# Optimization experiments

Hardware: AMD Instinct MI355X
Metric: run time of the kernel (lower is better)

## Reference

```python
import jax, jax.numpy as jnp
import numpy as np

BATCH, IN_DIM, N_HID, OUT_DIM = 8192, 1024, 2048, 256
EDGE_DENSITY = 0.05


def _make_mat():
    # adjacency with activation-type codes: 0=no edge, 1=w*x, 2=relu(w*x), 3=tanh(w*x), 4=sigmoid(w*x)
    rng = np.random.default_rng(0)
    n_rows, n_cols = N_HID + OUT_DIM, IN_DIM + N_HID
    mat = rng.integers(1, 5, size=(n_rows, n_cols)) * (rng.random((n_rows, n_cols)) < EDGE_DENSITY)
    mat[:N_HID, IN_DIM:] = 0  # hidden nodes read only from inputs (valid DAG instance of the loop)
    # guarantee every node has at least one incoming edge (original code assumes this)
    hz = np.where(mat[:N_HID, :IN_DIM].sum(1) == 0)[0]
    mat[hz, hz % IN_DIM] = 1
    oz = np.where(mat[N_HID:].sum(1) == 0)[0]
    mat[N_HID + oz, oz % n_cols] = 1
    return mat.astype(np.int32)


def setup_inputs() -> dict:
    key = jax.random.key(0)
    x = jax.random.normal(key, (BATCH, IN_DIM), dtype=jnp.float32)
    w = jnp.ones((), dtype=jnp.float32)  # constant_weight
    mat = jnp.asarray(_make_mat())
    return {"x": x, "w": w, "mat": mat}


_ACTS = [(1, lambda z: z), (2, jax.nn.relu), (3, jnp.tanh), (4, jax.nn.sigmoid)]


def _node_values(src, w, M):
    # src: [B, S] source node values; M: [R, S] activation-type codes
    # node_r = sum_s act_{M[r,s]}(w * src[:, s]) for M[r,s] != 0
    total = jnp.zeros((src.shape[0], M.shape[0]), dtype=src.dtype)
    ws = w * src
    for t, f in _ACTS:
        mask = (M == t).astype(src.dtype)  # [R, S]
        total = total + f(ws) @ mask.T
    return total


def reference(x, w, mat):
    in_dim = x.shape[1]
    num_hidden = mat.shape[1] - in_dim
    hidden = _node_values(x, w, mat[:num_hidden, :in_dim])          # [B, N_HID]
    src = jnp.concatenate([x, hidden], axis=1)                       # [B, IN+N_HID]
    outputs = _node_values(src, w, mat[num_hidden:, :])              # [B, OUT]
    return outputs
```

## Files before the change

kernel.cpp:

```cpp
#include <hip/hip_runtime.h>
#include <hip/hip_bf16.h>
#include <stdint.h>

#define BATCH   8192
#define IN_DIM  1024
#define N_HID   2048
#define OUT_DIM 256
#define SRC_DIM 3072

#define C     32
#define RB    16
#define BT    256
#define S1_CH (IN_DIM / C)
#define S1_RB (N_HID / RB)
#define S2_CH (SRC_DIM / C)
#define S2_RB (OUT_DIM / RB)
#define NSEG1 (S1_RB * S1_CH)
#define NSEG2 (S2_RB * S2_CH)
#define NCG2  16
#define ZSLOT 128
#define SEG_U32 160
#define ABUF_U32 ((4 * C + 1) * 128)


#define RFL(x) __builtin_amdgcn_readfirstlane((uint32_t)(x))

typedef _Float16 h2 __attribute__((ext_vector_type(2)));

__global__ void k_prep(const int* __restrict__ mat,
                       uint32_t* __restrict__ seg1, uint32_t* __restrict__ seg2,
                       uint32_t* __restrict__ hdr1, uint32_t* __restrict__ hdr2) {
    int wid  = (blockIdx.x * blockDim.x + threadIdx.x) >> 6;
    int lane = threadIdx.x & 63;
    if (wid >= NSEG1 + NSEG2) return;

    int row0, col0;
    uint32_t *seg, *hdr;
    if (wid < NSEG1) {
        int rb = wid / S1_CH, ch = wid % S1_CH;
        row0 = rb * RB;          col0 = ch * C;
        seg = seg1 + (size_t)wid * SEG_U32;  hdr = hdr1 + wid;
    } else {
        int s  = wid - NSEG1;
        int rb = s / S2_CH, ch = s % S2_CH;
        row0 = N_HID + rb * RB;  col0 = ch * C;
        seg = seg2 + (size_t)s * SEG_U32;    hdr = hdr2 + s;
    }

    int n = 0;
    if (lane < RB) {
        const int4* m4 = (const int4*)(mat + (size_t)(row0 + lane) * SRC_DIM + col0);
        uint8_t* sb = (uint8_t*)seg;
        #pragma unroll
        for (int cc = 0; cc < 8; cc++) {
            int4 q4 = m4[cc];
            int codes[4] = {q4.x, q4.y, q4.z, q4.w};
            #pragma unroll
            for (int k = 0; k < 4; k++) {
                int code = codes[k];
                if (code != 0) {
                    int c = cc * 4 + k;
                    uint8_t slot = (uint8_t)((code - 1) * C + c);
                    if (n < 2) {
                        sb[2 * lane + n] = slot;
                    } else {
                        int j  = n - 2;
                        int pl = j >> 1;
                        sb[(size_t)(8 + 9 * pl + 1 + (lane >> 1)) * 4
                           + (lane & 1) * 2 + (j & 1)] = slot;
                    }
                    n++;
                }
            }
        }
    }
    int m = n;
    #pragma unroll
    for (int d = 1; d < 64; d <<= 1) m = max(m, __shfl_xor(m, d));
    uint32_t Wv = (m <= 2) ? 1u : 1u + (uint32_t)((m - 1) >> 1);

    for (uint32_t p = 1; p < Wv; p++) {
        unsigned long long b = __ballot(n > (int)(2 * p));
        if (lane == 0) seg[8 + 9 * (p - 1)] = (uint32_t)(b & 0xFFFFu);
    }
    if (lane == 0) *hdr = Wv;
}

__global__ __launch_bounds__(256) void k_xt(const float* __restrict__ x,
                                            float* __restrict__ x_t) {
    __shared__ float t[64][65];
    const int b0 = blockIdx.x * 64, c0 = blockIdx.y * 64;
    {
        int r  = threadIdx.x >> 4;
        int cq = (threadIdx.x & 15) * 4;
        #pragma unroll
        for (int k = 0; k < 4; k++) {
            int rr = r + 16 * k;
            float4 v = *(const float4*)&x[(size_t)(b0 + rr) * IN_DIM + c0 + cq];
            t[rr][cq + 0] = v.x; t[rr][cq + 1] = v.y;
            t[rr][cq + 2] = v.z; t[rr][cq + 3] = v.w;
        }
    }
    __syncthreads();
    {
        int bq  = (threadIdx.x & 15) * 4;
        int cc0 = threadIdx.x >> 4;
        #pragma unroll
        for (int k = 0; k < 4; k++) {
            int cc = cc0 + 16 * k;
            float4 v;
            v.x = t[bq + 0][cc]; v.y = t[bq + 1][cc];
            v.z = t[bq + 2][cc]; v.w = t[bq + 3][cc];
            *(float4*)&x_t[(size_t)(c0 + cc) * BATCH + b0 + bq] = v;
        }
    }
}

__device__ __forceinline__ uint32_t pkh(float a, float b) {
    auto r = __builtin_amdgcn_cvt_pkrtz(a, b);
    return __builtin_bit_cast(uint32_t, r);
}

__device__ __forceinline__ float rcp_f(float x) { return __builtin_amdgcn_rcpf(x); }

__device__ __forceinline__ void write_acts4(uint32_t* As, int c, int lane, float4 v) {
    *(uint2*)&As[(size_t)(0 * C + c) * 128 + 2 * lane] =
        make_uint2(pkh(v.x, v.y), pkh(v.z, v.w));
    *(uint2*)&As[(size_t)(1 * C + c) * 128 + 2 * lane] =
        make_uint2(pkh(fmaxf(v.x, 0.0f), fmaxf(v.y, 0.0f)),
                   pkh(fmaxf(v.z, 0.0f), fmaxf(v.w, 0.0f)));
    float ex = __expf(-v.x), ey = __expf(-v.y);
    float ez = __expf(-v.z), ew = __expf(-v.w);
    float tx = fmaf(2.0f, rcp_f(fmaf(ex, ex, 1.0f)), -1.0f);
    float ty = fmaf(2.0f, rcp_f(fmaf(ey, ey, 1.0f)), -1.0f);
    float tz = fmaf(2.0f, rcp_f(fmaf(ez, ez, 1.0f)), -1.0f);
    float tw = fmaf(2.0f, rcp_f(fmaf(ew, ew, 1.0f)), -1.0f);
    *(uint2*)&As[(size_t)(2 * C + c) * 128 + 2 * lane] =
        make_uint2(pkh(tx, ty), pkh(tz, tw));
    float sx = rcp_f(1.0f + ex), sy = rcp_f(1.0f + ey);
    float sz = rcp_f(1.0f + ez), sw = rcp_f(1.0f + ew);
    *(uint2*)&As[(size_t)(3 * C + c) * 128 + 2 * lane] =
        make_uint2(pkh(sx, sy), pkh(sz, sw));
}

#define SLOT_ACC(R, S)                                                         \
    {                                                                          \
        uint2 q_ = *(const uint2*)&As[(size_t)(S) * 128 + 2 * lane];           \
        accA[R] += __builtin_bit_cast(h2, q_.x);                               \
        accB[R] += __builtin_bit_cast(h2, q_.y);                               \
    }

#define EDGE_PLANES(SEGBASE, WVAL)                                             \
    {                                                                          \
        const uint32_t* sp_ = (SEGBASE);                                       \
        _Pragma("unroll")                                                      \
        for (int i = 0; i < 8; i++) {                                          \
            uint32_t g = RFL(sp_[i]);                                          \
            SLOT_ACC(2 * i,     g & 255u)                                      \
            SLOT_ACC(2 * i,     (g >> 8) & 255u)                               \
            SLOT_ACC(2 * i + 1, (g >> 16) & 255u)                              \
            SLOT_ACC(2 * i + 1, g >> 24)                                       \
        }                                                                      \
        _Pragma("unroll 1")                                                    \
        for (uint32_t p = 1; p < (WVAL); p++) {                                \
            const uint32_t* pp_ = sp_ + 8 + 9 * (p - 1);                       \
            uint32_t mask = RFL(pp_[0]);                                       \
            _Pragma("unroll")                                                  \
            for (int r = 0; r < RB; r++) {                                     \
                if (mask & (1u << r)) {                                        \
                    uint32_t h_ = RFL(pp_[1 + (r >> 1)]);                      \
                    uint32_t u_ = (r & 1) ? (h_ >> 16) : h_;                   \
                    SLOT_ACC(r, u_ & 255u)                                     \
                    SLOT_ACC(r, (u_ >> 8) & 255u)                              \
                }                                                              \
            }                                                                  \
        }                                                                      \
    }

__global__ __launch_bounds__(1024, 8) void k_hid(const float* __restrict__ x_t,
                                                 const float* __restrict__ wp,
                                                 const uint32_t* __restrict__ seg1,
                                                 const uint32_t* __restrict__ hdr1,
                                                 uint16_t* __restrict__ hidden_t) {
    __shared__ uint32_t As[ABUF_U32];

    const float w  = wp[0];
    const int tile = blockIdx.x;
    const int cgh  = blockIdx.z;
    const int lane = threadIdx.x & 63;
    const int wv   = __builtin_amdgcn_readfirstlane(threadIdx.x >> 6);
    const int rb   = blockIdx.y * 16 + wv;
    const int b0   = tile * BT;
    const int c0   = cgh * (S1_CH / 2);

    if (threadIdx.x < 128) As[ZSLOT * 128 + threadIdx.x] = 0u;

    h2 accA[RB], accB[RB];
    const h2 hz = {(_Float16)0.0f, (_Float16)0.0f};
    #pragma unroll
    for (int r = 0; r < RB; r++) { accA[r] = hz; accB[r] = hz; }

    float4 v[2];
    #pragma unroll
    for (int j = 0; j < 2; j++) {
        int gcol = c0 * C + wv * 2 + j;
        const float2* xp = (const float2*)&x_t[(size_t)gcol * BATCH + b0];
        float2 u0 = xp[lane], u1 = xp[64 + lane];
        v[j] = make_float4(w * u0.x, w * u0.y, w * u1.x, w * u1.y);
    }

    #pragma unroll 1
    for (int cj = 0; cj < S1_CH / 2; cj++) {
        int ch = c0 + cj;
        __syncthreads();
        write_acts4(As, wv * 2 + 0, lane, v[0]);
        write_acts4(As, wv * 2 + 1, lane, v[1]);
        __syncthreads();
        if (cj + 1 < S1_CH / 2) {
            #pragma unroll
            for (int j = 0; j < 2; j++) {
                int gcol = (ch + 1) * C + wv * 2 + j;
                const float2* xp = (const float2*)&x_t[(size_t)gcol * BATCH + b0];
                float2 u0 = xp[lane], u1 = xp[64 + lane];
                v[j] = make_float4(w * u0.x, w * u0.y, w * u1.x, w * u1.y);
            }
        }
        int sidx = rb * S1_CH + ch;
        uint32_t W = RFL(hdr1[sidx]);
        EDGE_PLANES(seg1 + (size_t)sidx * SEG_U32, W)
    }

    uint16_t* hout = hidden_t + (size_t)cgh * N_HID * BATCH;
    const int row0 = rb * RB;
    #pragma unroll
    for (int r = 0; r < RB; r++) {
        *(uint32_t*)&hout[(size_t)(row0 + r) * BATCH + b0 + 2 * lane] =
            __builtin_bit_cast(uint32_t, accA[r]);
        *(uint32_t*)&hout[(size_t)(row0 + r) * BATCH + b0 + 128 + 2 * lane] =
            __builtin_bit_cast(uint32_t, accB[r]);
    }
}

__device__ __forceinline__ float4 load_src4(const float* __restrict__ x_t,
                                            const uint16_t* __restrict__ hidden_t,
                                            int gcol, int b0, int lane, float w) {
    if (gcol < IN_DIM) {
        const float2* xp = (const float2*)&x_t[(size_t)gcol * BATCH + b0];
        float2 u0 = xp[lane], u1 = xp[64 + lane];
        return make_float4(w * u0.x, w * u0.y, w * u1.x, w * u1.y);
    } else {
        const uint16_t* hp = hidden_t + (size_t)(gcol - IN_DIM) * BATCH + b0;
        const uint16_t* hq = hp + (size_t)N_HID * BATCH;
        uint32_t a0 = *(const uint32_t*)&hp[2 * lane];
        uint32_t a1 = *(const uint32_t*)&hp[128 + 2 * lane];
        uint32_t c0 = *(const uint32_t*)&hq[2 * lane];
        uint32_t c1 = *(const uint32_t*)&hq[128 + 2 * lane];
        h2 s0 = __builtin_bit_cast(h2, a0) + __builtin_bit_cast(h2, c0);
        h2 s1 = __builtin_bit_cast(h2, a1) + __builtin_bit_cast(h2, c1);
        return make_float4(w * (float)s0.x, w * (float)s0.y,
                           w * (float)s1.x, w * (float)s1.y);
    }
}

__global__ __launch_bounds__(1024, 8) void k_out(const float* __restrict__ x_t,
                                                 const uint16_t* __restrict__ hidden_t,
                                                 const float* __restrict__ wp,
                                                 const uint32_t* __restrict__ seg2,
                                                 const uint32_t* __restrict__ hdr2,
                                                 uint32_t* __restrict__ partials) {
    __shared__ uint32_t As[ABUF_U32];

    const float w  = wp[0];
    const int tile = blockIdx.x;
    const int cg   = blockIdx.y;
    const int lane = threadIdx.x & 63;
    const int wv   = __builtin_amdgcn_readfirstlane(threadIdx.x >> 6);
    const int b0   = tile * BT;
    const int nch  = S2_CH / NCG2;

    if (threadIdx.x < 128) As[ZSLOT * 128 + threadIdx.x] = 0u;

    h2 accA[RB], accB[RB];
    const h2 hz = {(_Float16)0.0f, (_Float16)0.0f};
    #pragma unroll
    for (int r = 0; r < RB; r++) { accA[r] = hz; accB[r] = hz; }

    float4 v[2];
    #pragma unroll
    for (int j = 0; j < 2; j++)
        v[j] = load_src4(x_t, hidden_t, (cg * nch) * C + wv * 2 + j, b0, lane, w);

    #pragma unroll 1
    for (int cj = 0; cj < nch; cj++) {
        int ch = cg * nch + cj;
        __syncthreads();
        write_acts4(As, wv * 2 + 0, lane, v[0]);
        write_acts4(As, wv * 2 + 1, lane, v[1]);
        __syncthreads();
        if (cj + 1 < nch) {
            #pragma unroll
            for (int j = 0; j < 2; j++)
                v[j] = load_src4(x_t, hidden_t, (ch + 1) * C + wv * 2 + j, b0, lane, w);
        }
        int sidx = wv * S2_CH + ch;
        uint32_t W = RFL(hdr2[sidx]);
        EDGE_PLANES(seg2 + (size_t)sidx * SEG_U32, W)
    }

    #pragma unroll
    for (int r = 0; r < RB; r++) {
        size_t base = ((size_t)cg * OUT_DIM + wv * RB + r) * (BATCH / 2) + (b0 >> 1);
        partials[base + lane]      = __builtin_bit_cast(uint32_t, accA[r]);
        partials[base + 64 + lane] = __builtin_bit_cast(uint32_t, accB[r]);
    }
}

__global__ __launch_bounds__(256) void k_sum(const uint32_t* __restrict__ partials,
                                             float* __restrict__ out) {
    __shared__ float t[16][130];
    const int b0 = blockIdx.x * 128, r0 = blockIdx.y * 16;
    const int lane = threadIdx.x & 63;
    const int g4   = threadIdx.x >> 6;

    #pragma unroll
    for (int k = 0; k < 4; k++) {
        int rr = g4 * 4 + k;
        float sx = 0.0f, sy = 0.0f;
        #pragma unroll
        for (int cg = 0; cg < NCG2; cg++) {
            uint32_t q = partials[((size_t)cg * OUT_DIM + r0 + rr) * (BATCH / 2)
                                  + (b0 >> 1) + lane];
            h2 h = __builtin_bit_cast(h2, q);
            sx += (float)h.x;
            sy += (float)h.y;
        }
        t[rr][2 * lane]     = sx;
        t[rr][2 * lane + 1] = sy;
    }
    __syncthreads();
    #pragma unroll
    for (int k = 0; k < 2; k++) {
        int idx = threadIdx.x + 256 * k;
        int bb = idx >> 2, rq = idx & 3;
        float4 v;
        v.x = t[rq * 4 + 0][bb];
        v.y = t[rq * 4 + 1][bb];
        v.z = t[rq * 4 + 2][bb];
        v.w = t[rq * 4 + 3][bb];
        *(float4*)&out[(size_t)(b0 + bb) * OUT_DIM + r0 + rq * 4] = v;
    }
}

extern "C" void kernel_launch(void* const* d_in, const int* in_sizes, int n_in,
                              void* d_out, int out_size, void* d_ws, size_t ws_size,
                              hipStream_t stream) {
    const float* x   = (const float*)d_in[0];
    const float* w   = (const float*)d_in[1];
    const int*   mat = (const int*)d_in[2];
    float* out = (float*)d_out;

    uint8_t* ws = (uint8_t*)d_ws;
    size_t off = 0;
    uint16_t* hidden_t = (uint16_t*)(ws + off);
    off += (size_t)2 * BATCH * N_HID * 2;
    float* x_t = (float*)(ws + off);        off += (size_t)IN_DIM * BATCH * 4;
    uint32_t* seg1 = (uint32_t*)(ws + off); off += (size_t)NSEG1 * SEG_U32 * 4;
    uint32_t* seg2 = (uint32_t*)(ws + off); off += (size_t)NSEG2 * SEG_U32 * 4;
    uint32_t* hdr1 = (uint32_t*)(ws + off); off += (size_t)NSEG1 * 4;
    uint32_t* hdr2 = (uint32_t*)(ws + off); off += (size_t)NSEG2 * 4;
    uint32_t* partials = (uint32_t*)(ws + off);
    off += (size_t)NCG2 * OUT_DIM * (BATCH / 2) * 4;
    (void)ws_size; (void)in_sizes; (void)n_in; (void)out_size;

    hipMemsetAsync(seg1, 0x80, (size_t)(NSEG1 + NSEG2) * SEG_U32 * 4, stream);

    {
        int nseg = NSEG1 + NSEG2;
        k_prep<<<(nseg + 3) / 4, 256, 0, stream>>>(mat, seg1, seg2, hdr1, hdr2);
    }
    {
        dim3 g(BATCH / 64, IN_DIM / 64);
        k_xt<<<g, 256, 0, stream>>>(x, x_t);
    }
    {
        dim3 g(BATCH / BT, 8, 2);
        k_hid<<<g, 1024, 0, stream>>>(x_t, w, seg1, hdr1, hidden_t);
    }
    {
        dim3 g(BATCH / BT, NCG2);
        k_out<<<g, 1024, 0, stream>>>(x_t, hidden_t, w, seg2, hdr2, partials);
    }
    {
        dim3 g(BATCH / 128, OUT_DIM / 16);
        k_sum<<<g, 256, 0, stream>>>(partials, out);
    }
}
```

Measured before the change: 238.7 us.

## Shrink dense edge prefix to one slot per row and build segments in LDS

The segment encoding now keeps only one guaranteed edge per row in the dense prefix (4 words instead of 8), and extra edges go into masked planes. This cuts the unconditional slot-accumulate work per segment in the hidden and output kernels, at the cost of more plane iterations for rows with two or more edges. The prep kernel now builds each segment in shared memory, with sentinel fill done there, and copies it out, which removes the separate memset launch.

```diff
diff --git a/kernel.cpp b/kernel.cpp
--- a/kernel.cpp
+++ b/kernel.cpp
@@ -27,10 +27,12 @@
 
 typedef _Float16 h2 __attribute__((ext_vector_type(2)));
 
-__global__ void k_prep(const int* __restrict__ mat,
+__global__ __launch_bounds__(256) void k_prep(const int* __restrict__ mat,
                        uint32_t* __restrict__ seg1, uint32_t* __restrict__ seg2,
                        uint32_t* __restrict__ hdr1, uint32_t* __restrict__ hdr2) {
+    __shared__ uint32_t lseg[4][SEG_U32];
     int wid  = (blockIdx.x * blockDim.x + threadIdx.x) >> 6;
+    int wv   = threadIdx.x >> 6;
     int lane = threadIdx.x & 63;
     if (wid >= NSEG1 + NSEG2) return;
 
@@ -47,10 +49,15 @@
         seg = seg2 + (size_t)s * SEG_U32;    hdr = hdr2 + s;
     }
 
+    uint32_t* ls = lseg[wv];
+    for (int k = lane; k < SEG_U32; k += 64) ls[k] = 0x80808080u;
+    __asm__ volatile("s_waitcnt lgkmcnt(0)" ::: "memory");
+    __builtin_amdgcn_sched_barrier(0);
+
     int n = 0;
     if (lane < RB) {
         const int4* m4 = (const int4*)(mat + (size_t)(row0 + lane) * SRC_DIM + col0);
-        uint8_t* sb = (uint8_t*)seg;
+        uint8_t* sb = (uint8_t*)ls;
         #pragma unroll
         for (int cc = 0; cc < 8; cc++) {
             int4 q4 = m4[cc];
@@ -61,13 +68,13 @@
                 if (code != 0) {
                     int c = cc * 4 + k;
                     uint8_t slot = (uint8_t)((code - 1) * C + c);
-                    if (n < 2) {
-                        sb[2 * lane + n] = slot;
+                    if (n == 0) {
+                        sb[lane] = slot;
                     } else {
-                        int j  = n - 2;
-                        int pl = j >> 1;
-                        sb[(size_t)(8 + 9 * pl + 1 + (lane >> 1)) * 4
-                           + (lane & 1) * 2 + (j & 1)] = slot;
+                        int jj = n - 1;
+                        int pl = jj >> 1;
+                        sb[(size_t)(4 + 9 * pl + 1 + (lane >> 1)) * 4
+                           + (lane & 1) * 2 + (jj & 1)] = slot;
                     }
                     n++;
                 }
@@ -77,12 +84,16 @@
     int m = n;
     #pragma unroll
     for (int d = 1; d < 64; d <<= 1) m = max(m, __shfl_xor(m, d));
-    uint32_t Wv = (m <= 2) ? 1u : 1u + (uint32_t)((m - 1) >> 1);
+    uint32_t Wv = 1u + (uint32_t)(m >> 1);
 
     for (uint32_t p = 1; p < Wv; p++) {
-        unsigned long long b = __ballot(n > (int)(2 * p));
-        if (lane == 0) seg[8 + 9 * (p - 1)] = (uint32_t)(b & 0xFFFFu);
-    }
+        unsigned long long b = __ballot(n >= (int)(2 * p));
+        if (lane == 0) ls[4 + 9 * (p - 1)] = (uint32_t)(b & 0xFFFFu);
+    }
+    __asm__ volatile("s_waitcnt lgkmcnt(0)" ::: "memory");
+    __builtin_amdgcn_sched_barrier(0);
+
+    for (int k = lane; k < SEG_U32; k += 64) seg[k] = ls[k];
     if (lane == 0) *hdr = Wv;
 }
 
@@ -154,16 +165,16 @@
     {                                                                          \
         const uint32_t* sp_ = (SEGBASE);                                       \
         _Pragma("unroll")                                                      \
-        for (int i = 0; i < 8; i++) {                                          \
+        for (int i = 0; i < 4; i++) {                                          \
             uint32_t g = RFL(sp_[i]);                                          \
-            SLOT_ACC(2 * i,     g & 255u)                                      \
-            SLOT_ACC(2 * i,     (g >> 8) & 255u)                               \
-            SLOT_ACC(2 * i + 1, (g >> 16) & 255u)                              \
-            SLOT_ACC(2 * i + 1, g >> 24)                                       \
+            SLOT_ACC(4 * i + 0, g & 255u)                                      \
+            SLOT_ACC(4 * i + 1, (g >> 8) & 255u)                               \
+            SLOT_ACC(4 * i + 2, (g >> 16) & 255u)                              \
+            SLOT_ACC(4 * i + 3, g >> 24)                                       \
         }                                                                      \
         _Pragma("unroll 1")                                                    \
         for (uint32_t p = 1; p < (WVAL); p++) {                                \
-            const uint32_t* pp_ = sp_ + 8 + 9 * (p - 1);                       \
+            const uint32_t* pp_ = sp_ + 4 + 9 * (p - 1);                       \
             uint32_t mask = RFL(pp_[0]);                                       \
             _Pragma("unroll")                                                  \
             for (int r = 0; r < RB; r++) {                                     \
@@ -372,8 +383,6 @@
     off += (size_t)NCG2 * OUT_DIM * (BATCH / 2) * 4;
     (void)ws_size; (void)in_sizes; (void)n_in; (void)out_size;
 
-    hipMemsetAsync(seg1, 0x80, (size_t)(NSEG1 + NSEG2) * SEG_U32 * 4, stream);
-
     {
         int nseg = NSEG1 + NSEG2;
         k_prep<<<(nseg + 3) / 4, 256, 0, stream>>>(mat, seg1, seg2, hdr1, hdr2);
```

After: 235.8 us. About the same (-1.2%).
